# Kernel optimization log

Measured on AMD Instinct MI355X. Metric: run time of the kernel, lower is better.

The kernel has to match this reference:

```python
import jax, jax.numpy as jnp
import numpy as np

B, H, M, N, D = 8, 8, 512, 512, 64
HID = 16
MIX1 = (1.0 / 2.0) ** 0.5
MIX2 = (1.0 / 16.0) ** 0.5


def setup_inputs() -> dict:
    key = jax.random.key(0)
    ks = jax.random.split(key, 8)
    q = jax.random.normal(ks[0], (B, H, M, D), dtype=jnp.float32)
    k = jax.random.normal(ks[1], (B, H, N, D), dtype=jnp.float32)
    v = jax.random.normal(ks[2], (B, H, N, D), dtype=jnp.float32)
    dmat = jax.random.uniform(ks[3], (B, M, N), dtype=jnp.float32)
    mix_W1 = jax.random.uniform(ks[4], (H, 2, HID), minval=-MIX1, maxval=MIX1, dtype=jnp.float32)
    mix_b1 = jax.random.uniform(ks[5], (H, HID), minval=-MIX1, maxval=MIX1, dtype=jnp.float32)
    mix_W2 = jax.random.uniform(ks[6], (H, HID, 1), minval=-MIX2, maxval=MIX2, dtype=jnp.float32)
    mix_b2 = jax.random.uniform(ks[7], (H, 1), minval=-MIX2, maxval=MIX2, dtype=jnp.float32)
    return {"q": q, "k": k, "v": v, "dmat": dmat,
            "mix_W1": mix_W1, "mix_b1": mix_b1, "mix_W2": mix_W2, "mix_b2": mix_b2}


def reference(q, k, v, dmat, mix_W1, mix_b1, mix_W2, mix_b2):
    # attention scores: [b,h,m,n]
    scale = 1.0 / jnp.sqrt(jnp.float32(k.shape[-1]))
    scores = jnp.einsum("bhmd,bhnd->bhmn", q, k) * scale
    # stack dot-product scores with distance matrix: [b,h,m,n,2]
    mixed = jnp.stack([scores, jnp.broadcast_to(dmat[:, None, :, :], scores.shape)], axis=-1)
    # per-head 2-layer MLP over the 2-channel axis
    h1 = jax.nn.relu(jnp.einsum("bhmnc,hcf->bhmnf", mixed, mix_W1)
                     + mix_b1[None, :, None, None, :])          # [b,h,m,n,HID]
    mixed_scores = (jnp.einsum("bhmnf,hfo->bhmno", h1, mix_W2)[..., 0]
                    + mix_b2[None, :, None, None, 0])            # [b,h,m,n]
    attn = jax.nn.softmax(mixed_scores, axis=-1)
    return jnp.einsum("bhmn,bhnd->bhmd", attn, v)
```

## Files before the change

### kernel.cpp

```cpp
#include <hip/hip_runtime.h>
#include <hip/hip_bf16.h>


typedef __attribute__((ext_vector_type(4))) float f32x4;
typedef __attribute__((ext_vector_type(8))) __bf16 bf16x8;
typedef __attribute__((ext_vector_type(4))) unsigned short us4;
typedef __attribute__((ext_vector_type(8))) unsigned short us8;

union U8 { us8 u; bf16x8 b; };

static __device__ __forceinline__ unsigned short bf_hi(float x) {
    unsigned int u = __float_as_uint(x);
    u += 0x7fffu + ((u >> 16) & 1u);
    return (unsigned short)(u >> 16);
}
static __device__ __forceinline__ float bf_f(unsigned short s) {
    return __uint_as_float(((unsigned int)s) << 16);
}
static __device__ __forceinline__ float rlf(float x) {
    return __uint_as_float(__builtin_amdgcn_readfirstlane(__float_as_uint(x)));
}

static __device__ __forceinline__ int sw64(int row, int col) {
    return row * 64 + ((((col >> 3) ^ (row & 7)) << 3) | (col & 7));
}
static __device__ __forceinline__ int swdm(int row, int col) {
    return row * 64 + ((((col >> 2) ^ (row & 15)) << 2) | (col & 3));
}

#define B_ 8
#define H_ 8
#define M_ 512
#define N_ 512
#define D_ 64
#define HID_ 16

__global__ __launch_bounds__(256, 2) void msdpa_kernel(
    const float* __restrict__ qg, const float* __restrict__ kg,
    const float* __restrict__ vg, const float* __restrict__ dg,
    const float* __restrict__ w1g, const float* __restrict__ b1g,
    const float* __restrict__ w2g, float* __restrict__ outg)
{
    extern __shared__ f32x4 smem4[];
    unsigned short* KH  = (unsigned short*)smem4;
    unsigned short* KL  = KH + 4096;
    unsigned short* VTH = KL + 4096;
    unsigned short* VTL = VTH + 4096;
    float*          DM  = (float*)(VTL + 4096);
    unsigned short* PH  = (unsigned short*)(DM + 4096);
    unsigned short* PL  = PH + 4096;

    const int tid  = threadIdx.x;
    const int lane = tid & 63;
    const int wv   = tid >> 6;
    const int r16  = lane & 15;
    const int g    = lane >> 4;

    const int bm = blockIdx.x;
    const int h  = blockIdx.y;
    const int b  = blockIdx.z;

    unsigned short* PHw = PH + wv * 1024;
    unsigned short* PLw = PL + wv * 1024;

    const float* w1h = w1g + h * 2 * HID_;
    const float* b1h = b1g + h * HID_;
    const float* w2h = w2g + h * HID_;
    float ap[HID_], cc[HID_], bb[HID_], wp[HID_];
#pragma unroll
    for (int f = 0; f < HID_; ++f) {
        ap[f] = rlf(w1h[f]) * 0.125f;
        cc[f] = rlf(w1h[HID_ + f]);
        bb[f] = rlf(b1h[f]);
        wp[f] = rlf(w2h[f]) * 1.4426950408889634f;
    }

    const long bh = (long)(b * H_ + h);
    const float* qbase = qg + (bh * M_ + (long)bm * 64 + wv * 16 + r16) * D_;
    bf16x8 qh[2], ql[2];
#pragma unroll
    for (int ks = 0; ks < 2; ++ks) {
        f32x4 x0 = *(const f32x4*)(qbase + ks * 32 + g * 8);
        f32x4 x1 = *(const f32x4*)(qbase + ks * 32 + g * 8 + 4);
        U8 uh, ul;
#pragma unroll
        for (int j = 0; j < 8; ++j) {
            float xv = (j < 4) ? x0[j] : x1[j - 4];
            unsigned short hs = bf_hi(xv);
            uh.u[j] = hs;
            ul.u[j] = bf_hi(xv - bf_f(hs));
        }
        qh[ks] = uh.b; ql[ks] = ul.b;
    }

    f32x4 oacc[4];
#pragma unroll
    for (int dt = 0; dt < 4; ++dt) oacc[dt] = f32x4{0.f, 0.f, 0.f, 0.f};
    float mrun = -1e30f, lsum = 0.0f;

    const float* kbase = kg + bh * N_ * D_;
    const float* vbase = vg + bh * N_ * D_;
    const float* dbase = dg + ((long)b * M_ + (long)bm * 64) * N_;

    for (int nt = 0; nt < 8; ++nt) {
        const int n0 = nt * 64;
        __syncthreads();
#pragma unroll
        for (int it = 0; it < 4; ++it) {
            int e  = it * 1024 + tid * 4;
            int rr = e >> 6, c0 = e & 63;
            f32x4 kk = *(const f32x4*)(kbase + (long)(n0 + rr) * D_ + c0);
            us4 khs, kls;
#pragma unroll
            for (int i = 0; i < 4; ++i) {
                unsigned short hs = bf_hi(kk[i]);
                khs[i] = hs; kls[i] = bf_hi(kk[i] - bf_f(hs));
            }
            int kidx = sw64(rr, c0);
            *(us4*)(KH + kidx) = khs;
            *(us4*)(KL + kidx) = kls;
            f32x4 vv = *(const f32x4*)(vbase + (long)(n0 + rr) * D_ + c0);
#pragma unroll
            for (int i = 0; i < 4; ++i) {
                unsigned short hs = bf_hi(vv[i]);
                VTH[sw64(c0 + i, rr)] = hs;
                VTL[sw64(c0 + i, rr)] = bf_hi(vv[i] - bf_f(hs));
            }
            f32x4 dd = *(const f32x4*)(dbase + (long)rr * N_ + n0 + c0);
            *(f32x4*)(DM + swdm(rr, c0)) = dd;
        }
        __syncthreads();

        f32x4 sacc[4];
#pragma unroll
        for (int n16 = 0; n16 < 4; ++n16) sacc[n16] = f32x4{0.f, 0.f, 0.f, 0.f};
#pragma unroll
        for (int n16 = 0; n16 < 4; ++n16) {
            int row = n16 * 16 + r16;
#pragma unroll
            for (int ks = 0; ks < 2; ++ks) {
                int off = sw64(row, ks * 32 + g * 8);
                bf16x8 kh_ = *(bf16x8*)(KH + off);
                bf16x8 kl_ = *(bf16x8*)(KL + off);
                sacc[n16] = __builtin_amdgcn_mfma_f32_16x16x32_bf16(kh_, qh[ks], sacc[n16], 0, 0, 0);
                sacc[n16] = __builtin_amdgcn_mfma_f32_16x16x32_bf16(kh_, ql[ks], sacc[n16], 0, 0, 0);
                sacc[n16] = __builtin_amdgcn_mfma_f32_16x16x32_bf16(kl_, qh[ks], sacc[n16], 0, 0, 0);
            }
        }

        const int dmrow = wv * 16 + r16;
        f32x4 dmv[4];
#pragma unroll
        for (int n16 = 0; n16 < 4; ++n16)
            dmv[n16] = *(const f32x4*)(DM + swdm(dmrow, n16 * 16 + g * 4));
        float ms[4][4];
#pragma unroll
        for (int n16 = 0; n16 < 4; ++n16)
#pragma unroll
            for (int r = 0; r < 4; ++r) ms[n16][r] = 0.0f;
#pragma unroll
        for (int f = 0; f < HID_; ++f) {
            float a = ap[f], c = cc[f], bcst = bb[f], w = wp[f];
#pragma unroll
            for (int n16 = 0; n16 < 4; ++n16)
#pragma unroll
                for (int r = 0; r < 4; ++r) {
                    float u = fmaf(a, sacc[n16][r], fmaf(c, dmv[n16][r], bcst));
                    ms[n16][r] = fmaf(w, fmaxf(u, 0.0f), ms[n16][r]);
                }
        }

        float mloc = -1e30f;
#pragma unroll
        for (int n16 = 0; n16 < 4; ++n16)
#pragma unroll
            for (int r = 0; r < 4; ++r) mloc = fmaxf(mloc, ms[n16][r]);
        mloc = fmaxf(mloc, __shfl_xor(mloc, 16));
        mloc = fmaxf(mloc, __shfl_xor(mloc, 32));
        float mnew = fmaxf(mrun, mloc);
        float sc = exp2f(mrun - mnew);
        mrun = mnew;

        float psum = 0.0f;
#pragma unroll
        for (int n16 = 0; n16 < 4; ++n16) {
            us4 phs, pls;
#pragma unroll
            for (int r = 0; r < 4; ++r) {
                float p = exp2f(ms[n16][r] - mnew);
                psum += p;
                unsigned short hs = bf_hi(p);
                phs[r] = hs;
                pls[r] = bf_hi(p - bf_f(hs));
            }
            int pidx = sw64(r16, n16 * 16 + g * 4);
            *(us4*)(PHw + pidx) = phs;
            *(us4*)(PLw + pidx) = pls;
        }
        lsum = lsum * sc + psum;

        float scm[4];
#pragma unroll
        for (int r = 0; r < 4; ++r) scm[r] = __shfl(sc, g * 4 + r);
#pragma unroll
        for (int dt = 0; dt < 4; ++dt)
#pragma unroll
            for (int r = 0; r < 4; ++r) oacc[dt][r] *= scm[r];

#pragma unroll
        for (int ks = 0; ks < 2; ++ks) {
            int poff = sw64(r16, ks * 32 + g * 8);
            bf16x8 pa = *(bf16x8*)(PHw + poff);
            bf16x8 pb = *(bf16x8*)(PLw + poff);
#pragma unroll
            for (int dt = 0; dt < 4; ++dt) {
                int voff = sw64(dt * 16 + r16, ks * 32 + g * 8);
                bf16x8 vh_ = *(bf16x8*)(VTH + voff);
                bf16x8 vl_ = *(bf16x8*)(VTL + voff);
                oacc[dt] = __builtin_amdgcn_mfma_f32_16x16x32_bf16(pa, vh_, oacc[dt], 0, 0, 0);
                oacc[dt] = __builtin_amdgcn_mfma_f32_16x16x32_bf16(pa, vl_, oacc[dt], 0, 0, 0);
                oacc[dt] = __builtin_amdgcn_mfma_f32_16x16x32_bf16(pb, vh_, oacc[dt], 0, 0, 0);
            }
        }
    }

    lsum += __shfl_xor(lsum, 16);
    lsum += __shfl_xor(lsum, 32);
    float linv[4];
#pragma unroll
    for (int r = 0; r < 4; ++r) linv[r] = 1.0f / __shfl(lsum, g * 4 + r);

    float* obase = outg + (bh * M_ + (long)bm * 64 + wv * 16) * D_;
#pragma unroll
    for (int dt = 0; dt < 4; ++dt)
#pragma unroll
        for (int r = 0; r < 4; ++r)
            obase[(g * 4 + r) * D_ + dt * 16 + r16] = oacc[dt][r] * linv[r];
}

extern "C" void kernel_launch(void* const* d_in, const int* in_sizes, int n_in,
                              void* d_out, int out_size, void* d_ws, size_t ws_size,
                              hipStream_t stream) {
    const float* q  = (const float*)d_in[0];
    const float* k  = (const float*)d_in[1];
    const float* v  = (const float*)d_in[2];
    const float* dm = (const float*)d_in[3];
    const float* w1 = (const float*)d_in[4];
    const float* b1 = (const float*)d_in[5];
    const float* w2 = (const float*)d_in[6];
    float* out = (float*)d_out;

    (void)hipFuncSetAttribute(reinterpret_cast<const void*>(msdpa_kernel),
                              hipFuncAttributeMaxDynamicSharedMemorySize, 65536);
    dim3 grid(M_ / 64, H_, B_);
    msdpa_kernel<<<grid, dim3(256), 65536, stream>>>(q, k, v, dm, w1, b1, w2, out);
}
```

Measured before the change: 156.1 us.

## Prefetch K/V tiles, load dmat directly, use transpose LDS reads and packed MLP math

```diff
diff --git a/kernel.cpp b/kernel.cpp
--- a/kernel.cpp
+++ b/kernel.cpp
@@ -3,29 +3,26 @@
 
 
 typedef __attribute__((ext_vector_type(4))) float f32x4;
+typedef __attribute__((ext_vector_type(2))) float f32x2;
 typedef __attribute__((ext_vector_type(8))) __bf16 bf16x8;
-typedef __attribute__((ext_vector_type(4))) unsigned short us4;
-typedef __attribute__((ext_vector_type(8))) unsigned short us8;
-
-union U8 { us8 u; bf16x8 b; };
-
-static __device__ __forceinline__ unsigned short bf_hi(float x) {
-    unsigned int u = __float_as_uint(x);
-    u += 0x7fffu + ((u >> 16) & 1u);
-    return (unsigned short)(u >> 16);
-}
-static __device__ __forceinline__ float bf_f(unsigned short s) {
-    return __uint_as_float(((unsigned int)s) << 16);
-}
+typedef __attribute__((ext_vector_type(4))) __bf16 bf16x4;
+
 static __device__ __forceinline__ float rlf(float x) {
     return __uint_as_float(__builtin_amdgcn_readfirstlane(__float_as_uint(x)));
 }
-
+static __device__ __forceinline__ void cvt2(float x, __bf16& h, __bf16& l) {
+    h = (__bf16)x;
+    l = (__bf16)(x - (float)h);
+}
 static __device__ __forceinline__ int sw64(int row, int col) {
     return row * 64 + ((((col >> 3) ^ (row & 7)) << 3) | (col & 7));
 }
-static __device__ __forceinline__ int swdm(int row, int col) {
-    return row * 64 + ((((col >> 2) ^ (row & 15)) << 2) | (col & 3));
+
+template<int OFF>
+static __device__ __forceinline__ bf16x4 trrd(unsigned base) {
+    bf16x4 d;
+    asm volatile("ds_read_b64_tr_b16 %0, %1 offset:%2" : "=v"(d) : "v"(base), "i"(OFF));
+    return d;
 }
 
 #define B_ 8
@@ -34,6 +31,44 @@
 #define N_ 512
 #define D_ 64
 #define HID_ 16
+#define PSTRIDE 68
+
+template<int KS>
+static __device__ __forceinline__ void pv_half(unsigned vaddr, const __bf16* PHw,
+                                               const __bf16* PLw, int r16, int g,
+                                               f32x4* oacc) {
+    const int off0 = r16 * PSTRIDE + (((KS * 8)     + g) ^ r16) * 4;
+    const int off1 = r16 * PSTRIDE + (((KS * 8) + 4 + g) ^ r16) * 4;
+    bf16x4 pa0 = *(const bf16x4*)(PHw + off0);
+    bf16x4 pa1 = *(const bf16x4*)(PHw + off1);
+    bf16x4 pb0 = *(const bf16x4*)(PLw + off0);
+    bf16x4 pb1 = *(const bf16x4*)(PLw + off1);
+    bf16x8 pa = __builtin_shufflevector(pa0, pa1, 0, 1, 2, 3, 4, 5, 6, 7);
+    bf16x8 pb = __builtin_shufflevector(pb0, pb1, 0, 1, 2, 3, 4, 5, 6, 7);
+
+    bf16x4 h0[4], h1[4], l0[4], l1[4];
+#define TRV(arr, BOFF)                      \
+    arr[0] = trrd<(BOFF)      >(vaddr);     \
+    arr[1] = trrd<(BOFF) + 128>(vaddr);     \
+    arr[2] = trrd<(BOFF) + 256>(vaddr);     \
+    arr[3] = trrd<(BOFF) + 384>(vaddr);
+    TRV(h0, KS * 4096)
+    TRV(h1, KS * 4096 + 2048)
+    TRV(l0, KS * 4096 + 8192)
+    TRV(l1, KS * 4096 + 10240)
+#undef TRV
+    asm volatile("s_waitcnt lgkmcnt(0)" ::: "memory");
+    __builtin_amdgcn_sched_barrier(0);
+
+#pragma unroll
+    for (int dt = 0; dt < 4; ++dt) {
+        bf16x8 vh = __builtin_shufflevector(h0[dt], h1[dt], 0, 1, 2, 3, 4, 5, 6, 7);
+        bf16x8 vl = __builtin_shufflevector(l0[dt], l1[dt], 0, 1, 2, 3, 4, 5, 6, 7);
+        oacc[dt] = __builtin_amdgcn_mfma_f32_16x16x32_bf16(pa, vh, oacc[dt], 0, 0, 0);
+        oacc[dt] = __builtin_amdgcn_mfma_f32_16x16x32_bf16(pa, vl, oacc[dt], 0, 0, 0);
+        oacc[dt] = __builtin_amdgcn_mfma_f32_16x16x32_bf16(pb, vh, oacc[dt], 0, 0, 0);
+    }
+}
 
 __global__ __launch_bounds__(256, 2) void msdpa_kernel(
     const float* __restrict__ qg, const float* __restrict__ kg,
@@ -41,14 +76,13 @@
     const float* __restrict__ w1g, const float* __restrict__ b1g,
     const float* __restrict__ w2g, float* __restrict__ outg)
 {
-    extern __shared__ f32x4 smem4[];
-    unsigned short* KH  = (unsigned short*)smem4;
-    unsigned short* KL  = KH + 4096;
-    unsigned short* VTH = KL + 4096;
-    unsigned short* VTL = VTH + 4096;
-    float*          DM  = (float*)(VTL + 4096);
-    unsigned short* PH  = (unsigned short*)(DM + 4096);
-    unsigned short* PL  = PH + 4096;
+    extern __shared__ __bf16 smem[];
+    __bf16* KH = smem;
+    __bf16* KL = KH + 4096;
+    __bf16* VH = KL + 4096;
+    __bf16* VL = VH + 4096;
+    __bf16* PH = VL + 4096;
+    __bf16* PL = PH + 4 * 16 * PSTRIDE;
 
     const int tid  = threadIdx.x;
     const int lane = tid & 63;
@@ -60,8 +94,8 @@
     const int h  = blockIdx.y;
     const int b  = blockIdx.z;
 
-    unsigned short* PHw = PH + wv * 1024;
-    unsigned short* PLw = PL + wv * 1024;
+    __bf16* PHw = PH + wv * 16 * PSTRIDE;
+    __bf16* PLw = PL + wv * 16 * PSTRIDE;
 
     const float* w1h = w1g + h * 2 * HID_;
     const float* b1h = b1g + h * HID_;
@@ -82,15 +116,14 @@
     for (int ks = 0; ks < 2; ++ks) {
         f32x4 x0 = *(const f32x4*)(qbase + ks * 32 + g * 8);
         f32x4 x1 = *(const f32x4*)(qbase + ks * 32 + g * 8 + 4);
-        U8 uh, ul;
-#pragma unroll
-        for (int j = 0; j < 8; ++j) {
-            float xv = (j < 4) ? x0[j] : x1[j - 4];
-            unsigned short hs = bf_hi(xv);
-            uh.u[j] = hs;
-            ul.u[j] = bf_hi(xv - bf_f(hs));
-        }
-        qh[ks] = uh.b; ql[ks] = ul.b;
+        bf16x8 hv, lv;
+#pragma unroll
+        for (int j = 0; j < 4; ++j) {
+            __bf16 hs, ls;
+            cvt2(x0[j], hs, ls); hv[j] = hs; lv[j] = ls;
+            cvt2(x1[j], hs, ls); hv[4 + j] = hs; lv[4 + j] = ls;
+        }
+        qh[ks] = hv; ql[ks] = lv;
     }
 
     f32x4 oacc[4];
@@ -98,48 +131,64 @@
     for (int dt = 0; dt < 4; ++dt) oacc[dt] = f32x4{0.f, 0.f, 0.f, 0.f};
     float mrun = -1e30f, lsum = 0.0f;
 
-    const float* kbase = kg + bh * N_ * D_;
-    const float* vbase = vg + bh * N_ * D_;
-    const float* dbase = dg + ((long)b * M_ + (long)bm * 64) * N_;
+    const float* kb  = kg + bh * N_ * D_;
+    const float* vb  = vg + bh * N_ * D_;
+    const float* dmp = dg + ((long)b * M_ + (long)bm * 64 + wv * 16 + r16) * N_ + g * 4;
+    const unsigned vhbase = (unsigned)(size_t)VH;
+    const unsigned vaddr  = vhbase + (unsigned)(g * 512 + r16 * 8);
+    const int e = tid * 4;
+
+    f32x4 kk[4], vv[4];
+#pragma unroll
+    for (int it = 0; it < 4; ++it) {
+        kk[it] = *(const f32x4*)(kb + it * 1024 + e);
+        vv[it] = *(const f32x4*)(vb + it * 1024 + e);
+    }
 
     for (int nt = 0; nt < 8; ++nt) {
         const int n0 = nt * 64;
         __syncthreads();
 #pragma unroll
         for (int it = 0; it < 4; ++it) {
-            int e  = it * 1024 + tid * 4;
-            int rr = e >> 6, c0 = e & 63;
-            f32x4 kk = *(const f32x4*)(kbase + (long)(n0 + rr) * D_ + c0);
-            us4 khs, kls;
+            const int ee = it * 1024 + e;
+            const int rr = ee >> 6, c0 = ee & 63;
+            bf16x4 kh4, kl4, vh4, vl4;
 #pragma unroll
             for (int i = 0; i < 4; ++i) {
-                unsigned short hs = bf_hi(kk[i]);
-                khs[i] = hs; kls[i] = bf_hi(kk[i] - bf_f(hs));
-            }
-            int kidx = sw64(rr, c0);
-            *(us4*)(KH + kidx) = khs;
-            *(us4*)(KL + kidx) = kls;
-            f32x4 vv = *(const f32x4*)(vbase + (long)(n0 + rr) * D_ + c0);
-#pragma unroll
-            for (int i = 0; i < 4; ++i) {
-                unsigned short hs = bf_hi(vv[i]);
-                VTH[sw64(c0 + i, rr)] = hs;
-                VTL[sw64(c0 + i, rr)] = bf_hi(vv[i] - bf_f(hs));
-            }
-            f32x4 dd = *(const f32x4*)(dbase + (long)rr * N_ + n0 + c0);
-            *(f32x4*)(DM + swdm(rr, c0)) = dd;
+                __bf16 hs, ls;
+                cvt2(kk[it][i], hs, ls); kh4[i] = hs; kl4[i] = ls;
+                cvt2(vv[it][i], hs, ls); vh4[i] = hs; vl4[i] = ls;
+            }
+            const int kidx = sw64(rr, c0);
+            *(bf16x4*)(KH + kidx) = kh4;
+            *(bf16x4*)(KL + kidx) = kl4;
+            const int vidx = ((rr >> 2) * 4 + (c0 >> 4)) * 64 + (rr & 3) * 16 + (c0 & 15);
+            *(bf16x4*)(VH + vidx) = vh4;
+            *(bf16x4*)(VL + vidx) = vl4;
         }
         __syncthreads();
 
+        if (nt < 7) {
+#pragma unroll
+            for (int it = 0; it < 4; ++it) {
+                kk[it] = *(const f32x4*)(kb + (n0 + 64) * 64 + it * 1024 + e);
+                vv[it] = *(const f32x4*)(vb + (n0 + 64) * 64 + it * 1024 + e);
+            }
+        }
+        f32x4 dmv[4];
+#pragma unroll
+        for (int n16 = 0; n16 < 4; ++n16)
+            dmv[n16] = *(const f32x4*)(dmp + n0 + n16 * 16);
+
         f32x4 sacc[4];
 #pragma unroll
         for (int n16 = 0; n16 < 4; ++n16) sacc[n16] = f32x4{0.f, 0.f, 0.f, 0.f};
 #pragma unroll
         for (int n16 = 0; n16 < 4; ++n16) {
-            int row = n16 * 16 + r16;
+            const int row = n16 * 16 + r16;
 #pragma unroll
             for (int ks = 0; ks < 2; ++ks) {
-                int off = sw64(row, ks * 32 + g * 8);
+                const int off = sw64(row, ks * 32 + g * 8);
                 bf16x8 kh_ = *(bf16x8*)(KH + off);
                 bf16x8 kl_ = *(bf16x8*)(KL + off);
                 sacc[n16] = __builtin_amdgcn_mfma_f32_16x16x32_bf16(kh_, qh[ks], sacc[n16], 0, 0, 0);
@@ -148,54 +197,58 @@
             }
         }
 
-        const int dmrow = wv * 16 + r16;
-        f32x4 dmv[4];
-#pragma unroll
-        for (int n16 = 0; n16 < 4; ++n16)
-            dmv[n16] = *(const f32x4*)(DM + swdm(dmrow, n16 * 16 + g * 4));
-        float ms[4][4];
-#pragma unroll
-        for (int n16 = 0; n16 < 4; ++n16)
-#pragma unroll
-            for (int r = 0; r < 4; ++r) ms[n16][r] = 0.0f;
+        f32x2 sp[8], dp[8], acc2[8];
+#pragma unroll
+        for (int n16 = 0; n16 < 4; ++n16) {
+            sp[2 * n16]     = f32x2{sacc[n16][0], sacc[n16][1]};
+            sp[2 * n16 + 1] = f32x2{sacc[n16][2], sacc[n16][3]};
+            dp[2 * n16]     = f32x2{dmv[n16][0], dmv[n16][1]};
+            dp[2 * n16 + 1] = f32x2{dmv[n16][2], dmv[n16][3]};
+        }
+#pragma unroll
+        for (int p = 0; p < 8; ++p) acc2[p] = f32x2{0.f, 0.f};
+        const f32x2 zz = f32x2{0.f, 0.f};
 #pragma unroll
         for (int f = 0; f < HID_; ++f) {
-            float a = ap[f], c = cc[f], bcst = bb[f], w = wp[f];
-#pragma unroll
-            for (int n16 = 0; n16 < 4; ++n16)
-#pragma unroll
-                for (int r = 0; r < 4; ++r) {
-                    float u = fmaf(a, sacc[n16][r], fmaf(c, dmv[n16][r], bcst));
-                    ms[n16][r] = fmaf(w, fmaxf(u, 0.0f), ms[n16][r]);
-                }
-        }
-
-        float mloc = -1e30f;
-#pragma unroll
-        for (int n16 = 0; n16 < 4; ++n16)
-#pragma unroll
-            for (int r = 0; r < 4; ++r) mloc = fmaxf(mloc, ms[n16][r]);
+            const f32x2 av = f32x2{ap[f], ap[f]};
+            const f32x2 cv = f32x2{cc[f], cc[f]};
+            const f32x2 bv = f32x2{bb[f], bb[f]};
+            const f32x2 wv2 = f32x2{wp[f], wp[f]};
+#pragma unroll
+            for (int p = 0; p < 8; ++p) {
+                f32x2 u = cv * dp[p] + bv;
+                u = av * sp[p] + u;
+                u = __builtin_elementwise_max(u, zz);
+                acc2[p] = wv2 * u + acc2[p];
+            }
+        }
+
+        f32x2 mx = acc2[0];
+#pragma unroll
+        for (int p = 1; p < 8; ++p) mx = __builtin_elementwise_max(mx, acc2[p]);
+        float mloc = fmaxf(mx[0], mx[1]);
         mloc = fmaxf(mloc, __shfl_xor(mloc, 16));
         mloc = fmaxf(mloc, __shfl_xor(mloc, 32));
-        float mnew = fmaxf(mrun, mloc);
-        float sc = exp2f(mrun - mnew);
+        const float mnew = fmaxf(mrun, mloc);
+        const float sc = exp2f(mrun - mnew);
         mrun = mnew;
 
         float psum = 0.0f;
 #pragma unroll
         for (int n16 = 0; n16 < 4; ++n16) {
-            us4 phs, pls;
+            bf16x4 ph4, pl4;
 #pragma unroll
             for (int r = 0; r < 4; ++r) {
-                float p = exp2f(ms[n16][r] - mnew);
+                const float p = exp2f(acc2[2 * n16 + (r >> 1)][r & 1] - mnew);
                 psum += p;
-                unsigned short hs = bf_hi(p);
-                phs[r] = hs;
-                pls[r] = bf_hi(p - bf_f(hs));
-            }
-            int pidx = sw64(r16, n16 * 16 + g * 4);
-            *(us4*)(PHw + pidx) = phs;
-            *(us4*)(PLw + pidx) = pls;
+                __bf16 hs, ls;
+                cvt2(p, hs, ls);
+                ph4[r] = hs; pl4[r] = ls;
+            }
+            const int c = (n16 * 4 + g) ^ r16;
+            const int off = r16 * PSTRIDE + c * 4;
+            *(bf16x4*)(PHw + off) = ph4;
+            *(bf16x4*)(PLw + off) = pl4;
         }
         lsum = lsum * sc + psum;
 
@@ -207,21 +260,8 @@
 #pragma unroll
             for (int r = 0; r < 4; ++r) oacc[dt][r] *= scm[r];
 
-#pragma unroll
-        for (int ks = 0; ks < 2; ++ks) {
-            int poff = sw64(r16, ks * 32 + g * 8);
-            bf16x8 pa = *(bf16x8*)(PHw + poff);
-            bf16x8 pb = *(bf16x8*)(PLw + poff);
-#pragma unroll
-            for (int dt = 0; dt < 4; ++dt) {
-                int voff = sw64(dt * 16 + r16, ks * 32 + g * 8);
-                bf16x8 vh_ = *(bf16x8*)(VTH + voff);
-                bf16x8 vl_ = *(bf16x8*)(VTL + voff);
-                oacc[dt] = __builtin_amdgcn_mfma_f32_16x16x32_bf16(pa, vh_, oacc[dt], 0, 0, 0);
-                oacc[dt] = __builtin_amdgcn_mfma_f32_16x16x32_bf16(pa, vl_, oacc[dt], 0, 0, 0);
-                oacc[dt] = __builtin_amdgcn_mfma_f32_16x16x32_bf16(pb, vh_, oacc[dt], 0, 0, 0);
-            }
-        }
+        pv_half<0>(vaddr, PHw, PLw, r16, g, oacc);
+        pv_half<1>(vaddr, PHw, PLw, r16, g, oacc);
     }
 
     lsum += __shfl_xor(lsum, 16);
@@ -253,5 +293,5 @@
     (void)hipFuncSetAttribute(reinterpret_cast<const void*>(msdpa_kernel),
                               hipFuncAttributeMaxDynamicSharedMemorySize, 65536);
     dim3 grid(M_ / 64, H_, B_);
-    msdpa_kernel<<<grid, dim3(256), 65536, stream>>>(q, k, v, dm, w1, b1, w2, out);
-}
+    msdpa_kernel<<<grid, dim3(256), 50176, stream>>>(q, k, v, dm, w1, b1, w2, out);
+}
```

Result: faster. 136.7 us (-12.4%).
